# Kernel tuning notes

Measured on AMD Instinct MI355X. Metric: run time of the kernel, lower is better.

Reference implementation:

```python
import jax, jax.numpy as jnp
import numpy as np


def setup_inputs() -> dict:
    key = jax.random.key(0)
    ks = jax.random.split(key, 9)
    b, h, w, c = 32, 64, 64, 256
    s = 0.02  # small init to mimic variance-scaled NIN weights
    return {
        "x": jax.random.normal(ks[0], (b, h, w, c), dtype=jnp.float32),
        "Wq": jax.random.normal(ks[1], (c, c), dtype=jnp.float32) * s,
        "bq": jnp.zeros((c,), dtype=jnp.float32),
        "Wk": jax.random.normal(ks[2], (c, c), dtype=jnp.float32) * s,
        "bk": jnp.zeros((c,), dtype=jnp.float32),
        "Wv": jax.random.normal(ks[3], (c, c), dtype=jnp.float32) * s,
        "bv": jnp.zeros((c,), dtype=jnp.float32),
        "Wo": jax.random.normal(ks[4], (c, c), dtype=jnp.float32) * s,
        "bo": jnp.zeros((c,), dtype=jnp.float32),
    }


def reference(x, Wq, bq, Wk, bk, Wv, bv, Wo, bo):
    # x: [b, h, w, c]. NOTE: in the source, GroupNorm(x) is computed but its
    # output is immediately overwritten (dead code); Q/K/V come from raw x.
    b, h, w, c = x.shape
    cf = jnp.asarray(c, x.dtype)
    Q = jnp.einsum('bhwc,cd->bhwd', x, Wq) + bq
    K = jnp.einsum('bhwc,cd->bhwd', x, Wk) + bk
    V = jnp.einsum('bhwc,cd->bhwd', x, Wv) + bv
    # per-row attention over the W axis: scores [b, h, w, w]
    # double scaling: /(c*sqrt(1/2)) then softmax(./sqrt(c))
    scores = jnp.einsum('bhic,bhjc->bhij', Q, K) / (cf * jnp.sqrt(jnp.asarray(0.5, x.dtype)))
    attn = jax.nn.softmax(scores / jnp.sqrt(cf), axis=-1)
    out = jnp.einsum('bhij,bhjc->bhic', attn, V)
    out = jnp.einsum('bhwc,cd->bhwd', out, Wo) + bo
    return out + x
```

## Files before the change

### kernel.cpp

```cpp
#include <hip/hip_runtime.h>
#include <hip/hip_bf16.h>
#include <stdint.h>


typedef __bf16 bf16x8 __attribute__((ext_vector_type(8)));
typedef __bf16 bf16x4 __attribute__((ext_vector_type(4)));
typedef float f32x4 __attribute__((ext_vector_type(4)));

#define C 256
#define WTOK 64
#define CP 264
#define VP 72
#define PP 72

__device__ __bf16 g_wt[4 * 65536];

__device__ __forceinline__ bf16x8 ld8(const __bf16* p) {
  return *reinterpret_cast<const bf16x8*>(p);
}

__global__ __launch_bounds__(256) void wtrans_kernel(
    const float* __restrict__ wq, const float* __restrict__ wk,
    const float* __restrict__ wv, const float* __restrict__ wo) {
  __shared__ __bf16 tile[32][33];
  const float* src = (blockIdx.z == 0) ? wq : (blockIdx.z == 1) ? wk
                    : (blockIdx.z == 2) ? wv : wo;
  __bf16* d = &g_wt[0] + (size_t)blockIdx.z * 65536;
  const int tx = threadIdx.x, ty = threadIdx.y;
  const int x = blockIdx.x * 32 + tx;
  const int y0 = blockIdx.y * 32;
  for (int i = 0; i < 4; ++i)
    tile[ty + 8 * i][tx] = (__bf16)src[(size_t)(y0 + ty + 8 * i) * 256 + x];
  __syncthreads();
  const int xt = blockIdx.y * 32 + tx;
  const int yt0 = blockIdx.x * 32;
  for (int i = 0; i < 4; ++i)
    d[(size_t)(yt0 + ty + 8 * i) * 256 + xt] = tile[tx][ty + 8 * i];
}

template <int MODE>
__device__ __forceinline__ void proj_tile(const __bf16* __restrict__ asrc,
                                          const __bf16* __restrict__ w,
                                          const float* __restrict__ bias,
                                          __bf16* __restrict__ dst,
                                          int nb, int quad, int l16) {
  f32x4 D[4][4];
  const f32x4 zero = {0.f, 0.f, 0.f, 0.f};
  for (int m = 0; m < 4; ++m)
    for (int nt = 0; nt < 4; ++nt) D[m][nt] = zero;
  for (int kc = 0; kc < 8; ++kc) {
    const int ko = kc * 32 + quad * 8;
    bf16x8 a[4];
    for (int m = 0; m < 4; ++m) a[m] = ld8(asrc + (m * 16 + l16) * CP + ko);
    for (int nt = 0; nt < 4; ++nt) {
      bf16x8 b = ld8(w + (size_t)(nb + nt * 16 + l16) * 256 + ko);
      for (int m = 0; m < 4; ++m)
        D[m][nt] = __builtin_amdgcn_mfma_f32_16x16x32_bf16(a[m], b, D[m][nt], 0, 0, 0);
    }
  }
  float bs[4];
  for (int nt = 0; nt < 4; ++nt) bs[nt] = bias[nb + nt * 16 + l16];
  for (int m = 0; m < 4; ++m)
    for (int nt = 0; nt < 4; ++nt)
      for (int r = 0; r < 4; ++r) {
        const int tok = m * 16 + quad * 4 + r;
        const int ch = nb + nt * 16 + l16;
        const float v = D[m][nt][r] + bs[nt];
        if (MODE == 0) dst[tok * CP + ch] = (__bf16)v;
        else dst[ch * VP + tok] = (__bf16)v;
      }
}

__global__ __launch_bounds__(256, 1) void attn_fused_kernel(
    const float* __restrict__ x,
    const float* __restrict__ bq, const float* __restrict__ bk,
    const float* __restrict__ bv, const float* __restrict__ bo,
    float* __restrict__ out) {
  __shared__ __align__(16) __bf16 smem[56832];
  __bf16* xs = smem;
  __bf16* qs = smem + 16896;
  __bf16* ks = smem + 16896 + 16896;
  __bf16* vt = smem + 16896;
  __bf16* os = smem + 16896 + 18432;
  __bf16* ps = smem + 52224;

  const int tid = threadIdx.x;
  const int wv = tid >> 6;
  const int lane = tid & 63;
  const int quad = lane >> 4;
  const int l16 = lane & 15;
  const int bh = blockIdx.x;
  const float* xrow = x + (size_t)bh * (WTOK * C);

  for (int it = 0; it < 16; ++it) {
    const int chunk = tid + it * 256;
    const int row = chunk >> 6;
    const int c4 = (chunk & 63) << 2;
    const float4 v = *reinterpret_cast<const float4*>(xrow + row * 256 + c4);
    bf16x4 b;
    b[0] = (__bf16)v.x; b[1] = (__bf16)v.y; b[2] = (__bf16)v.z; b[3] = (__bf16)v.w;
    *reinterpret_cast<bf16x4*>(xs + row * CP + c4) = b;
  }
  __syncthreads();

  const int nb = wv * 64;
  const __bf16* wtq = g_wt;
  const __bf16* wtk = g_wt + 65536;
  const __bf16* wtv = g_wt + 131072;
  const __bf16* wto = g_wt + 196608;

  proj_tile<0>(xs, wtq, bq, qs, nb, quad, l16);
  proj_tile<0>(xs, wtk, bk, ks, nb, quad, l16);
  __syncthreads();

  const int i0 = wv * 16;
  f32x4 S[4];
  {
    const f32x4 zero = {0.f, 0.f, 0.f, 0.f};
    for (int nt = 0; nt < 4; ++nt) S[nt] = zero;
    bf16x8 qa[8];
    for (int kc = 0; kc < 8; ++kc)
      qa[kc] = ld8(qs + (i0 + l16) * CP + kc * 32 + quad * 8);
    for (int nt = 0; nt < 4; ++nt)
      for (int kc = 0; kc < 8; ++kc) {
        bf16x8 kb = ld8(ks + (nt * 16 + l16) * CP + kc * 32 + quad * 8);
        S[nt] = __builtin_amdgcn_mfma_f32_16x16x32_bf16(qa[kc], kb, S[nt], 0, 0, 0);
      }
  }
  __syncthreads();

  const float SCALE = 1.0f / (256.0f * 16.0f * 0.70710678118654752f);
  float p[4][4], invs[4];
  for (int r = 0; r < 4; ++r) {
    float mx = -1e30f;
    for (int nt = 0; nt < 4; ++nt) {
      const float s = S[nt][r] * SCALE;
      p[nt][r] = s;
      mx = fmaxf(mx, s);
    }
    for (int msk = 1; msk < 16; msk <<= 1) mx = fmaxf(mx, __shfl_xor(mx, msk));
    float sum = 0.f;
    for (int nt = 0; nt < 4; ++nt) {
      const float e = __expf(p[nt][r] - mx);
      p[nt][r] = e;
      sum += e;
    }
    for (int msk = 1; msk < 16; msk <<= 1) sum += __shfl_xor(sum, msk);
    invs[r] = 1.0f / sum;
    for (int nt = 0; nt < 4; ++nt)
      ps[(i0 + quad * 4 + r) * PP + nt * 16 + l16] = (__bf16)p[nt][r];
  }

  proj_tile<1>(xs, wtv, bv, vt, nb, quad, l16);
  __syncthreads();

  f32x4 O[16];
  {
    const f32x4 zero = {0.f, 0.f, 0.f, 0.f};
    for (int ct = 0; ct < 16; ++ct) O[ct] = zero;
    bf16x8 pa[2];
    for (int kc = 0; kc < 2; ++kc)
      pa[kc] = ld8(ps + (i0 + l16) * PP + kc * 32 + quad * 8);
    for (int ct = 0; ct < 16; ++ct)
      for (int kc = 0; kc < 2; ++kc) {
        bf16x8 vb = ld8(vt + (ct * 16 + l16) * VP + kc * 32 + quad * 8);
        O[ct] = __builtin_amdgcn_mfma_f32_16x16x32_bf16(pa[kc], vb, O[ct], 0, 0, 0);
      }
  }
  for (int ct = 0; ct < 16; ++ct)
    for (int r = 0; r < 4; ++r)
      os[(i0 + quad * 4 + r) * CP + ct * 16 + l16] = (__bf16)(O[ct][r] * invs[r]);
  __syncthreads();

  {
    f32x4 D[4][4];
    const f32x4 zero = {0.f, 0.f, 0.f, 0.f};
    for (int m = 0; m < 4; ++m)
      for (int nt = 0; nt < 4; ++nt) D[m][nt] = zero;
    for (int kc = 0; kc < 8; ++kc) {
      const int ko = kc * 32 + quad * 8;
      bf16x8 a[4];
      for (int m = 0; m < 4; ++m) a[m] = ld8(os + (m * 16 + l16) * CP + ko);
      for (int nt = 0; nt < 4; ++nt) {
        bf16x8 b = ld8(wto + (size_t)(nb + nt * 16 + l16) * 256 + ko);
        for (int m = 0; m < 4; ++m)
          D[m][nt] = __builtin_amdgcn_mfma_f32_16x16x32_bf16(a[m], b, D[m][nt], 0, 0, 0);
      }
    }
    float bs[4];
    for (int nt = 0; nt < 4; ++nt) bs[nt] = bo[nb + nt * 16 + l16];
    for (int m = 0; m < 4; ++m)
      for (int nt = 0; nt < 4; ++nt)
        for (int r = 0; r < 4; ++r) {
          const int tok = m * 16 + quad * 4 + r;
          const int ch = nb + nt * 16 + l16;
          const float v = D[m][nt][r] + bs[nt] + xrow[tok * 256 + ch];
          out[((size_t)bh * WTOK + tok) * C + ch] = v;
        }
  }
}

extern "C" void kernel_launch(void* const* d_in, const int* in_sizes, int n_in,
                              void* d_out, int out_size, void* d_ws, size_t ws_size,
                              hipStream_t stream) {
  (void)in_sizes; (void)n_in; (void)out_size; (void)d_ws; (void)ws_size;
  const float* x  = (const float*)d_in[0];
  const float* Wq = (const float*)d_in[1];
  const float* bq = (const float*)d_in[2];
  const float* Wk = (const float*)d_in[3];
  const float* bk = (const float*)d_in[4];
  const float* Wv = (const float*)d_in[5];
  const float* bv = (const float*)d_in[6];
  const float* Wo = (const float*)d_in[7];
  const float* bo = (const float*)d_in[8];
  float* out = (float*)d_out;

  hipLaunchKernelGGL(wtrans_kernel, dim3(8, 8, 4), dim3(32, 8, 1), 0, stream,
                     Wq, Wk, Wv, Wo);
  hipLaunchKernelGGL(attn_fused_kernel, dim3(2048), dim3(256), 0, stream,
                     x, bq, bk, bv, bo, out);
}
```

Baseline: 425.9 us.

## Fold Wq·Wkᵀ and Wv·Wo into combined weights to cut per-row GEMMs

Precomputes Wqk = Wq·Wkᵀ and Wvo = Wv·Wo, plus folded bias terms, in small setup kernels. Attention then runs as (x·Wqk)·xᵀ and (P·x)·Wvo, so the fused kernel does two 256x256 projections per row block instead of four. Dropping the bk term is valid because it is constant along each softmax row. Shared memory shrinks enough to allow two blocks per CU. The cost is three extra setup launches with a naive fp32 fold, and an uncoalesced strided fp32 read of x from global memory to build the P·x operand.

```diff
diff --git a/kernel.cpp b/kernel.cpp
--- a/kernel.cpp
+++ b/kernel.cpp
@@ -10,79 +10,73 @@
 #define C 256
 #define WTOK 64
 #define CP 264
-#define VP 72
 #define PP 72
 
-__device__ __bf16 g_wt[4 * 65536];
+__device__ float  g_wT[3 * 65536];
+__device__ __bf16 g_wqk[65536];
+__device__ __bf16 g_wvo[65536];
+__device__ float  g_c[256];
+__device__ float  g_bvo[256];
 
 __device__ __forceinline__ bf16x8 ld8(const __bf16* p) {
   return *reinterpret_cast<const bf16x8*>(p);
 }
 
-__global__ __launch_bounds__(256) void wtrans_kernel(
+__global__ __launch_bounds__(256) void trans_kernel(
     const float* __restrict__ wq, const float* __restrict__ wk,
-    const float* __restrict__ wv, const float* __restrict__ wo) {
-  __shared__ __bf16 tile[32][33];
-  const float* src = (blockIdx.z == 0) ? wq : (blockIdx.z == 1) ? wk
-                    : (blockIdx.z == 2) ? wv : wo;
-  __bf16* d = &g_wt[0] + (size_t)blockIdx.z * 65536;
+    const float* __restrict__ wv) {
+  __shared__ float tile[32][33];
+  const float* src = (blockIdx.z == 0) ? wq : (blockIdx.z == 1) ? wk : wv;
+  float* d = &g_wT[0] + (size_t)blockIdx.z * 65536;
   const int tx = threadIdx.x, ty = threadIdx.y;
-  const int x = blockIdx.x * 32 + tx;
-  const int y0 = blockIdx.y * 32;
+  const int k0 = blockIdx.x * 32;
+  const int m0 = blockIdx.y * 32;
   for (int i = 0; i < 4; ++i)
-    tile[ty + 8 * i][tx] = (__bf16)src[(size_t)(y0 + ty + 8 * i) * 256 + x];
-  __syncthreads();
-  const int xt = blockIdx.y * 32 + tx;
-  const int yt0 = blockIdx.x * 32;
+    tile[ty + 8 * i][tx] = src[(size_t)(k0 + ty + 8 * i) * 256 + m0 + tx];
+  __syncthreads();
   for (int i = 0; i < 4; ++i)
-    d[(size_t)(yt0 + ty + 8 * i) * 256 + xt] = tile[tx][ty + 8 * i];
-}
-
-template <int MODE>
-__device__ __forceinline__ void proj_tile(const __bf16* __restrict__ asrc,
-                                          const __bf16* __restrict__ w,
-                                          const float* __restrict__ bias,
-                                          __bf16* __restrict__ dst,
-                                          int nb, int quad, int l16) {
-  f32x4 D[4][4];
-  const f32x4 zero = {0.f, 0.f, 0.f, 0.f};
-  for (int m = 0; m < 4; ++m)
-    for (int nt = 0; nt < 4; ++nt) D[m][nt] = zero;
-  for (int kc = 0; kc < 8; ++kc) {
-    const int ko = kc * 32 + quad * 8;
-    bf16x8 a[4];
-    for (int m = 0; m < 4; ++m) a[m] = ld8(asrc + (m * 16 + l16) * CP + ko);
-    for (int nt = 0; nt < 4; ++nt) {
-      bf16x8 b = ld8(w + (size_t)(nb + nt * 16 + l16) * 256 + ko);
-      for (int m = 0; m < 4; ++m)
-        D[m][nt] = __builtin_amdgcn_mfma_f32_16x16x32_bf16(a[m], b, D[m][nt], 0, 0, 0);
-    }
-  }
-  float bs[4];
-  for (int nt = 0; nt < 4; ++nt) bs[nt] = bias[nb + nt * 16 + l16];
-  for (int m = 0; m < 4; ++m)
-    for (int nt = 0; nt < 4; ++nt)
-      for (int r = 0; r < 4; ++r) {
-        const int tok = m * 16 + quad * 4 + r;
-        const int ch = nb + nt * 16 + l16;
-        const float v = D[m][nt][r] + bs[nt];
-        if (MODE == 0) dst[tok * CP + ch] = (__bf16)v;
-        else dst[ch * VP + tok] = (__bf16)v;
-      }
-}
-
-__global__ __launch_bounds__(256, 1) void attn_fused_kernel(
-    const float* __restrict__ x,
-    const float* __restrict__ bq, const float* __restrict__ bk,
-    const float* __restrict__ bv, const float* __restrict__ bo,
-    float* __restrict__ out) {
-  __shared__ __align__(16) __bf16 smem[56832];
+    d[(size_t)(m0 + ty + 8 * i) * 256 + k0 + tx] = tile[tx][ty + 8 * i];
+}
+
+__global__ __launch_bounds__(256) void fold_kernel(
+    const float* __restrict__ wk, const float* __restrict__ wo) {
+  const int n = blockIdx.x;
+  const int k = threadIdx.x;
+  float acc = 0.f;
+  if (blockIdx.y == 0) {
+    const float* a = &g_wT[0];
+    #pragma unroll 8
+    for (int m = 0; m < 256; ++m) acc += a[m * 256 + k] * wk[n * 256 + m];
+    g_wqk[n * 256 + k] = (__bf16)acc;
+  } else {
+    const float* a = &g_wT[2 * 65536];
+    #pragma unroll 8
+    for (int m = 0; m < 256; ++m) acc += a[m * 256 + k] * wo[m * 256 + n];
+    g_wvo[n * 256 + k] = (__bf16)acc;
+  }
+}
+
+__global__ __launch_bounds__(256) void bias_kernel(
+    const float* __restrict__ bq, const float* __restrict__ bv,
+    const float* __restrict__ bo, const float* __restrict__ wo) {
+  const int n = threadIdx.x;
+  const float* wkT = &g_wT[65536];
+  float c = 0.f, bb = bo[n];
+  #pragma unroll 8
+  for (int m = 0; m < 256; ++m) c += bq[m] * wkT[m * 256 + n];
+  #pragma unroll 8
+  for (int k = 0; k < 256; ++k) bb += bv[k] * wo[k * 256 + n];
+  g_c[n] = c;
+  g_bvo[n] = bb;
+}
+
+__global__ __launch_bounds__(256, 2) void attn_fused_kernel(
+    const float* __restrict__ x, float* __restrict__ out) {
+  __shared__ __align__(16) __bf16 smem[38400];
   __bf16* xs = smem;
-  __bf16* qs = smem + 16896;
-  __bf16* ks = smem + 16896 + 16896;
-  __bf16* vt = smem + 16896;
-  __bf16* os = smem + 16896 + 18432;
-  __bf16* ps = smem + 52224;
+  __bf16* ts = smem + 16896;
+  __bf16* ys = ts;
+  __bf16* ps = smem + 33792;
 
   const int tid = threadIdx.x;
   const int wv = tid >> 6;
@@ -104,73 +98,7 @@
   __syncthreads();
 
   const int nb = wv * 64;
-  const __bf16* wtq = g_wt;
-  const __bf16* wtk = g_wt + 65536;
-  const __bf16* wtv = g_wt + 131072;
-  const __bf16* wto = g_wt + 196608;
-
-  proj_tile<0>(xs, wtq, bq, qs, nb, quad, l16);
-  proj_tile<0>(xs, wtk, bk, ks, nb, quad, l16);
-  __syncthreads();
-
   const int i0 = wv * 16;
-  f32x4 S[4];
-  {
-    const f32x4 zero = {0.f, 0.f, 0.f, 0.f};
-    for (int nt = 0; nt < 4; ++nt) S[nt] = zero;
-    bf16x8 qa[8];
-    for (int kc = 0; kc < 8; ++kc)
-      qa[kc] = ld8(qs + (i0 + l16) * CP + kc * 32 + quad * 8);
-    for (int nt = 0; nt < 4; ++nt)
-      for (int kc = 0; kc < 8; ++kc) {
-        bf16x8 kb = ld8(ks + (nt * 16 + l16) * CP + kc * 32 + quad * 8);
-        S[nt] = __builtin_amdgcn_mfma_f32_16x16x32_bf16(qa[kc], kb, S[nt], 0, 0, 0);
-      }
-  }
-  __syncthreads();
-
-  const float SCALE = 1.0f / (256.0f * 16.0f * 0.70710678118654752f);
-  float p[4][4], invs[4];
-  for (int r = 0; r < 4; ++r) {
-    float mx = -1e30f;
-    for (int nt = 0; nt < 4; ++nt) {
-      const float s = S[nt][r] * SCALE;
-      p[nt][r] = s;
-      mx = fmaxf(mx, s);
-    }
-    for (int msk = 1; msk < 16; msk <<= 1) mx = fmaxf(mx, __shfl_xor(mx, msk));
-    float sum = 0.f;
-    for (int nt = 0; nt < 4; ++nt) {
-      const float e = __expf(p[nt][r] - mx);
-      p[nt][r] = e;
-      sum += e;
-    }
-    for (int msk = 1; msk < 16; msk <<= 1) sum += __shfl_xor(sum, msk);
-    invs[r] = 1.0f / sum;
-    for (int nt = 0; nt < 4; ++nt)
-      ps[(i0 + quad * 4 + r) * PP + nt * 16 + l16] = (__bf16)p[nt][r];
-  }
-
-  proj_tile<1>(xs, wtv, bv, vt, nb, quad, l16);
-  __syncthreads();
-
-  f32x4 O[16];
-  {
-    const f32x4 zero = {0.f, 0.f, 0.f, 0.f};
-    for (int ct = 0; ct < 16; ++ct) O[ct] = zero;
-    bf16x8 pa[2];
-    for (int kc = 0; kc < 2; ++kc)
-      pa[kc] = ld8(ps + (i0 + l16) * PP + kc * 32 + quad * 8);
-    for (int ct = 0; ct < 16; ++ct)
-      for (int kc = 0; kc < 2; ++kc) {
-        bf16x8 vb = ld8(vt + (ct * 16 + l16) * VP + kc * 32 + quad * 8);
-        O[ct] = __builtin_amdgcn_mfma_f32_16x16x32_bf16(pa[kc], vb, O[ct], 0, 0, 0);
-      }
-  }
-  for (int ct = 0; ct < 16; ++ct)
-    for (int r = 0; r < 4; ++r)
-      os[(i0 + quad * 4 + r) * CP + ct * 16 + l16] = (__bf16)(O[ct][r] * invs[r]);
-  __syncthreads();
 
   {
     f32x4 D[4][4];
@@ -180,22 +108,107 @@
     for (int kc = 0; kc < 8; ++kc) {
       const int ko = kc * 32 + quad * 8;
       bf16x8 a[4];
-      for (int m = 0; m < 4; ++m) a[m] = ld8(os + (m * 16 + l16) * CP + ko);
+      for (int m = 0; m < 4; ++m) a[m] = ld8(xs + (m * 16 + l16) * CP + ko);
       for (int nt = 0; nt < 4; ++nt) {
-        bf16x8 b = ld8(wto + (size_t)(nb + nt * 16 + l16) * 256 + ko);
+        bf16x8 b = ld8(g_wqk + (size_t)(nb + nt * 16 + l16) * 256 + ko);
         for (int m = 0; m < 4; ++m)
           D[m][nt] = __builtin_amdgcn_mfma_f32_16x16x32_bf16(a[m], b, D[m][nt], 0, 0, 0);
       }
     }
+    float cs[4];
+    for (int nt = 0; nt < 4; ++nt) cs[nt] = g_c[nb + nt * 16 + l16];
+    for (int m = 0; m < 4; ++m)
+      for (int nt = 0; nt < 4; ++nt)
+        for (int r = 0; r < 4; ++r)
+          ts[(m * 16 + quad * 4 + r) * CP + nb + nt * 16 + l16] =
+              (__bf16)(D[m][nt][r] + cs[nt]);
+  }
+  __syncthreads();
+
+  f32x4 S[4];
+  {
+    const f32x4 zero = {0.f, 0.f, 0.f, 0.f};
+    for (int nt = 0; nt < 4; ++nt) S[nt] = zero;
+    bf16x8 qa[8];
+    for (int kc = 0; kc < 8; ++kc)
+      qa[kc] = ld8(ts + (i0 + l16) * CP + kc * 32 + quad * 8);
+    for (int nt = 0; nt < 4; ++nt)
+      for (int kc = 0; kc < 8; ++kc) {
+        bf16x8 kb = ld8(xs + (nt * 16 + l16) * CP + kc * 32 + quad * 8);
+        S[nt] = __builtin_amdgcn_mfma_f32_16x16x32_bf16(qa[kc], kb, S[nt], 0, 0, 0);
+      }
+  }
+
+  const float SCALE = 1.0f / (256.0f * 16.0f * 0.70710678118654752f);
+  for (int r = 0; r < 4; ++r) {
+    float p[4];
+    float mx = -1e30f;
+    for (int nt = 0; nt < 4; ++nt) {
+      p[nt] = S[nt][r] * SCALE;
+      mx = fmaxf(mx, p[nt]);
+    }
+    for (int msk = 1; msk < 16; msk <<= 1) mx = fmaxf(mx, __shfl_xor(mx, msk));
+    float sum = 0.f;
+    for (int nt = 0; nt < 4; ++nt) {
+      p[nt] = __expf(p[nt] - mx);
+      sum += p[nt];
+    }
+    for (int msk = 1; msk < 16; msk <<= 1) sum += __shfl_xor(sum, msk);
+    const float invs = 1.0f / sum;
+    for (int nt = 0; nt < 4; ++nt)
+      ps[(i0 + quad * 4 + r) * PP + nt * 16 + l16] = (__bf16)(p[nt] * invs);
+  }
+  __syncthreads();
+
+  {
+    f32x4 Y[16];
+    const f32x4 zero = {0.f, 0.f, 0.f, 0.f};
+    for (int ct = 0; ct < 16; ++ct) Y[ct] = zero;
+    bf16x8 pa[2];
+    for (int kc = 0; kc < 2; ++kc)
+      pa[kc] = ld8(ps + (i0 + l16) * PP + kc * 32 + quad * 8);
+    for (int ct = 0; ct < 16; ++ct) {
+      const int ch = ct * 16 + l16;
+      for (int kc = 0; kc < 2; ++kc) {
+        bf16x8 xb;
+        #pragma unroll
+        for (int jj = 0; jj < 8; ++jj) {
+          const int j = kc * 32 + quad * 8 + jj;
+          xb[jj] = (__bf16)xrow[j * 256 + ch];
+        }
+        Y[ct] = __builtin_amdgcn_mfma_f32_16x16x32_bf16(pa[kc], xb, Y[ct], 0, 0, 0);
+      }
+    }
+    for (int ct = 0; ct < 16; ++ct)
+      for (int r = 0; r < 4; ++r)
+        ys[(i0 + quad * 4 + r) * CP + ct * 16 + l16] = (__bf16)Y[ct][r];
+  }
+  __syncthreads();
+
+  {
+    f32x4 D[4][4];
+    const f32x4 zero = {0.f, 0.f, 0.f, 0.f};
+    for (int m = 0; m < 4; ++m)
+      for (int nt = 0; nt < 4; ++nt) D[m][nt] = zero;
+    for (int kc = 0; kc < 8; ++kc) {
+      const int ko = kc * 32 + quad * 8;
+      bf16x8 a[4];
+      for (int m = 0; m < 4; ++m) a[m] = ld8(ys + (m * 16 + l16) * CP + ko);
+      for (int nt = 0; nt < 4; ++nt) {
+        bf16x8 b = ld8(g_wvo + (size_t)(nb + nt * 16 + l16) * 256 + ko);
+        for (int m = 0; m < 4; ++m)
+          D[m][nt] = __builtin_amdgcn_mfma_f32_16x16x32_bf16(a[m], b, D[m][nt], 0, 0, 0);
+      }
+    }
     float bs[4];
-    for (int nt = 0; nt < 4; ++nt) bs[nt] = bo[nb + nt * 16 + l16];
+    for (int nt = 0; nt < 4; ++nt) bs[nt] = g_bvo[nb + nt * 16 + l16];
     for (int m = 0; m < 4; ++m)
       for (int nt = 0; nt < 4; ++nt)
         for (int r = 0; r < 4; ++r) {
           const int tok = m * 16 + quad * 4 + r;
           const int ch = nb + nt * 16 + l16;
-          const float v = D[m][nt][r] + bs[nt] + xrow[tok * 256 + ch];
-          out[((size_t)bh * WTOK + tok) * C + ch] = v;
+          out[((size_t)bh * WTOK + tok) * C + ch] =
+              D[m][nt][r] + bs[nt] + xrow[tok * 256 + ch];
         }
   }
 }
@@ -208,15 +221,14 @@
   const float* Wq = (const float*)d_in[1];
   const float* bq = (const float*)d_in[2];
   const float* Wk = (const float*)d_in[3];
-  const float* bk = (const float*)d_in[4];
   const float* Wv = (const float*)d_in[5];
   const float* bv = (const float*)d_in[6];
   const float* Wo = (const float*)d_in[7];
   const float* bo = (const float*)d_in[8];
   float* out = (float*)d_out;
 
-  hipLaunchKernelGGL(wtrans_kernel, dim3(8, 8, 4), dim3(32, 8, 1), 0, stream,
-                     Wq, Wk, Wv, Wo);
-  hipLaunchKernelGGL(attn_fused_kernel, dim3(2048), dim3(256), 0, stream,
-                     x, bq, bk, bv, bo, out);
-}
+  hipLaunchKernelGGL(trans_kernel, dim3(8, 8, 3), dim3(32, 8, 1), 0, stream, Wq, Wk, Wv);
+  hipLaunchKernelGGL(fold_kernel, dim3(256, 2, 1), dim3(256), 0, stream, Wk, Wo);
+  hipLaunchKernelGGL(bias_kernel, dim3(1), dim3(256), 0, stream, bq, bv, bo, Wo);
+  hipLaunchKernelGGL(attn_fused_kernel, dim3(2048), dim3(256), 0, stream, x, out);
+}
```

After: 370.3 us. 1.15x faster.
